# Performance work log

Hardware: AMD Instinct MI355X
Metric: run time of the kernel (lower is better)

The kernel has to match this reference:

```python
import jax, jax.numpy as jnp
import numpy as np

HEADS = 12
DIM_HEAD = 64
SCALE = DIM_HEAD ** -0.5


def setup_inputs() -> dict:
    key = jax.random.key(0)
    k1, k2, k3 = jax.random.split(key, 3)
    B, N, D = 4, 2048, 768
    inner = HEADS * DIM_HEAD  # 768
    x = jax.random.normal(k1, (B, N, D), dtype=jnp.float32)
    W_qkv = jax.random.normal(k2, (D, 3 * inner), dtype=jnp.float32) * (D ** -0.5)
    W_out = jax.random.normal(k3, (inner, D), dtype=jnp.float32) * (inner ** -0.5)
    b_out = jnp.zeros((D,), dtype=jnp.float32)
    return {"x": x, "W_qkv": W_qkv, "W_out": W_out, "b_out": b_out}


def reference(x, W_qkv, W_out, b_out):
    B, N, D = x.shape
    qkv = x @ W_qkv  # [B, N, 3*inner]
    q, k, v = jnp.split(qkv, 3, axis=-1)
    # 'b n (h d) -> b h n d'
    def split_heads(t):
        return t.reshape(B, N, HEADS, DIM_HEAD).transpose(0, 2, 1, 3)
    q, k, v = split_heads(q), split_heads(k), split_heads(v)
    dots = jnp.einsum('bhnd,bhmd->bhnm', q, k) * SCALE  # [B, H, N, N]
    attn = jax.nn.softmax(dots, axis=-1)
    out = jnp.einsum('bhnm,bhmd->bhnd', attn, v)
    out = out.transpose(0, 2, 1, 3).reshape(B, N, HEADS * DIM_HEAD)  # 'b h n d -> b n (h d)'
    return out @ W_out + b_out
```

## Files before the change

### kernel.cpp

```cpp
#include <hip/hip_runtime.h>
#include <hip/hip_bf16.h>

typedef __bf16 bf16_t;
typedef __bf16 bf16x4 __attribute__((ext_vector_type(4)));
typedef __bf16 bf16x8 __attribute__((ext_vector_type(8)));
typedef float f32x4 __attribute__((ext_vector_type(4)));
typedef float f32x16 __attribute__((ext_vector_type(16)));
typedef unsigned int u32x4 __attribute__((ext_vector_type(4)));

#define HEADS 12
#define DHEAD 64
#define NSEQ 2048
#define BATCH 4
#define DMODEL 768
#define NINNER 768

#define QSCALE 0.18033688011112042f

__device__ __forceinline__ void gl_lds16(const bf16_t* g, bf16_t* l) {
  __builtin_amdgcn_global_load_lds(
      (const __attribute__((address_space(1))) void*)g,
      (__attribute__((address_space(3))) void*)l, 16, 0, 0);
}

__device__ __forceinline__ unsigned pack_bf16_2(float a, float b) {
  unsigned lo = (unsigned)__builtin_bit_cast(unsigned short, (bf16_t)a);
  unsigned hi = (unsigned)__builtin_bit_cast(unsigned short, (bf16_t)b);
  return lo | (hi << 16);
}

__global__ void cast_bf16_kernel(const float* __restrict__ in, bf16_t* __restrict__ out, int n8) {
  int i = blockIdx.x * blockDim.x + threadIdx.x;
  const int stride = gridDim.x * blockDim.x;
  for (; i < n8; i += stride) {
    const f32x4* p = (const f32x4*)(in + (size_t)i * 8);
    f32x4 a = p[0], b = p[1];
    bf16x8 o;
#pragma unroll
    for (int j = 0; j < 4; ++j) { o[j] = (bf16_t)a[j]; o[j + 4] = (bf16_t)b[j]; }
    *(bf16x8*)(out + (size_t)i * 8) = o;
  }
}

__global__ void transpose_cast_kernel(const float* __restrict__ in, bf16_t* __restrict__ out,
                                      int K, int N) {
  __shared__ float tile[32][33];
  const int bx = blockIdx.x * 32;
  const int by = blockIdx.y * 32;
  const int tx = threadIdx.x, ty = threadIdx.y;
#pragma unroll
  for (int i = ty; i < 32; i += 8)
    tile[i][tx] = in[(size_t)(by + i) * N + bx + tx];
  __syncthreads();
#pragma unroll
  for (int i = ty; i < 32; i += 8)
    out[(size_t)(bx + i) * K + by + tx] = (bf16_t)tile[tx][i];
}

template <int MODE>
__global__ __launch_bounds__(256, 2)
void gemm_bt(const bf16_t* __restrict__ A, const bf16_t* __restrict__ Bt,
             bf16_t* __restrict__ qw, bf16_t* __restrict__ kw, bf16_t* __restrict__ vtw,
             const float* __restrict__ bias, float* __restrict__ outf,
             int M, int Nn, int K) {
  __shared__ bf16_t As[128 * 64];
  __shared__ bf16_t Bs[128 * 64];
  const int tid = threadIdx.x;
  const int wid = tid >> 6;
  const int lane = tid & 63;
  const int m0 = blockIdx.x * 128;
  const int n0 = blockIdx.y * 128;
  const int arow = lane >> 3;
  const int acol = (lane & 7) * 8;
  const int wm = (wid >> 1) * 64;
  const int wn = (wid & 1) * 64;
  const int fr = lane & 15;
  const int fg = lane >> 4;

  f32x4 acc[4][4] = {};

  for (int kt = 0; kt < K; kt += 64) {
    __syncthreads();
#pragma unroll
    for (int i = 0; i < 4; ++i) {
      const int c = i * 4 + wid;
      gl_lds16(A + (size_t)(m0 + c * 8 + arow) * K + kt + acol, As + c * 512);
      gl_lds16(Bt + (size_t)(n0 + c * 8 + arow) * K + kt + acol, Bs + c * 512);
    }
    __syncthreads();
#pragma unroll
    for (int kk = 0; kk < 2; ++kk) {
      bf16x8 af[4], bfr[4];
#pragma unroll
      for (int mi = 0; mi < 4; ++mi)
        af[mi] = *(const bf16x8*)(As + (wm + mi * 16 + fr) * 64 + kk * 32 + fg * 8);
#pragma unroll
      for (int ni = 0; ni < 4; ++ni)
        bfr[ni] = *(const bf16x8*)(Bs + (wn + ni * 16 + fr) * 64 + kk * 32 + fg * 8);
#pragma unroll
      for (int mi = 0; mi < 4; ++mi)
#pragma unroll
        for (int ni = 0; ni < 4; ++ni)
          acc[mi][ni] = __builtin_amdgcn_mfma_f32_16x16x32_bf16(af[mi], bfr[ni], acc[mi][ni], 0, 0, 0);
    }
  }

  if (MODE == 0 && n0 >= 2 * NINNER) {
#pragma unroll
    for (int mi = 0; mi < 4; ++mi) {
#pragma unroll
      for (int ni = 0; ni < 4; ++ni) {
        const int col = n0 + wn + ni * 16 + fr - 2 * NINNER;
        const int h = col >> 6, d = col & 63;
        const int row0 = m0 + wm + mi * 16 + fg * 4;
        const int b = row0 >> 11, n = row0 & 2047;
        bf16x4 pk;
#pragma unroll
        for (int r = 0; r < 4; ++r) pk[r] = (bf16_t)acc[mi][ni][r];
        *(bf16x4*)(vtw + ((size_t)((b * HEADS + h) * DHEAD + d)) * NSEQ + n) = pk;
      }
    }
  } else {
#pragma unroll
    for (int mi = 0; mi < 4; ++mi) {
#pragma unroll
      for (int ni = 0; ni < 4; ++ni) {
#pragma unroll
        for (int r = 0; r < 4; ++r) {
          const int row = m0 + wm + mi * 16 + fg * 4 + r;
          const int col = n0 + wn + ni * 16 + fr;
          float val = acc[mi][ni][r];
          if (MODE == 0) {
            const int which = col / NINNER;
            const int cin = col - which * NINNER;
            const int h = cin >> 6, d = cin & 63;
            const int b = row >> 11, n = row & 2047;
            bf16_t* dst = (which == 0) ? qw : kw;
            if (which == 0) val *= QSCALE;
            dst[(((size_t)(b * HEADS + h)) * NSEQ + n) * DHEAD + d] = (bf16_t)val;
          } else {
            outf[(size_t)row * Nn + col] = val + bias[col];
          }
        }
      }
    }
  }
}

__global__ __launch_bounds__(256, 3)
void attn_fwd(const bf16_t* __restrict__ qg, const bf16_t* __restrict__ kg,
              const bf16_t* __restrict__ vtg, bf16_t* __restrict__ og) {
  __shared__ bf16_t KV[2][16 * 512];
  const int tid = threadIdx.x, wid = tid >> 6, lane = tid & 63;
  const int logical = (blockIdx.x & 7) * 96 + (blockIdx.x >> 3);
  const int bh = logical >> 4;
  const int qbase = (logical & 15) * 128 + wid * 32;
  const bf16_t* Q = qg + (size_t)bh * NSEQ * DHEAD;
  const bf16_t* K = kg + (size_t)bh * NSEQ * DHEAD;
  const bf16_t* Vt = vtg + (size_t)bh * NSEQ * DHEAD;
  const int l31 = lane & 31, hi = lane >> 5;

  bf16x8 qf[4];
#pragma unroll
  for (int ks = 0; ks < 4; ++ks)
    qf[ks] = *(const bf16x8*)(Q + (size_t)(qbase + l31) * DHEAD + ks * 16 + hi * 8);

  f32x16 oacc[2] = {};
  float lsum = 0.f;

  auto stage = [&](int bsel, int t) {
    const int kv0 = t * 64;
#pragma unroll
    for (int i = 0; i < 4; ++i) {
      const int c = wid * 4 + i;
      bf16_t* dst = &KV[bsel][c * 512];
      if (c < 8) {
        gl_lds16(K + (size_t)(kv0 + (c >> 2) * 32 + l31) * DHEAD + (c & 3) * 16 + hi * 8, dst);
      } else {
        gl_lds16(Vt + (size_t)(((c >> 2) & 1) * 32 + l31) * NSEQ + kv0 + (c & 3) * 16 + hi * 8, dst);
      }
    }
  };

  stage(0, 0);

  for (int t = 0; t < NSEQ / 64; ++t) {
    const int buf = t & 1;
    asm volatile("s_waitcnt vmcnt(0) lgkmcnt(0)" ::: "memory");
    __builtin_amdgcn_sched_barrier(0);
    __syncthreads();
    if (t + 1 < NSEQ / 64) stage(buf ^ 1, t + 1);

    const bf16_t* base = &KV[buf][0];

    f32x16 sacc[2] = {};
    __builtin_amdgcn_s_setprio(1);
#pragma unroll
    for (int mi = 0; mi < 2; ++mi)
#pragma unroll
      for (int ks = 0; ks < 4; ++ks) {
        bf16x8 kf = *(const bf16x8*)(base + (mi * 4 + ks) * 512 + lane * 8);
        sacc[mi] = __builtin_amdgcn_mfma_f32_32x32x16_bf16(kf, qf[ks], sacc[mi], 0, 0, 0);
      }
    __builtin_amdgcn_s_setprio(0);

    bf16x8 pa[4];
#pragma unroll
    for (int mi = 0; mi < 2; ++mi) {
      float p[16];
#pragma unroll
      for (int r = 0; r < 16; ++r) p[r] = __builtin_amdgcn_exp2f(sacc[mi][r]);
      float rs = 0.f;
#pragma unroll
      for (int r = 0; r < 16; r += 4)
        rs += ((p[r] + p[r + 1]) + (p[r + 2] + p[r + 3]));
      lsum += rs;
      unsigned W[8];
#pragma unroll
      for (int j = 0; j < 8; ++j) W[j] = pack_bf16_2(p[2 * j], p[2 * j + 1]);
#pragma unroll
      for (int s = 0; s < 2; ++s) {
        const unsigned sendA = hi ? W[4 * s] : W[4 * s + 2];
        const unsigned sendB = hi ? W[4 * s + 1] : W[4 * s + 3];
        const unsigned recvA = __shfl_xor(sendA, 32, 64);
        const unsigned recvB = __shfl_xor(sendB, 32, 64);
        u32x4 pw;
        pw[0] = hi ? recvA : W[4 * s];
        pw[1] = hi ? recvB : W[4 * s + 1];
        pw[2] = hi ? W[4 * s + 2] : recvA;
        pw[3] = hi ? W[4 * s + 3] : recvB;
        pa[mi * 2 + s] = __builtin_bit_cast(bf16x8, pw);
      }
    }

    __builtin_amdgcn_s_setprio(1);
#pragma unroll
    for (int ni = 0; ni < 2; ++ni)
#pragma unroll
      for (int ks = 0; ks < 4; ++ks) {
        bf16x8 vf = *(const bf16x8*)(base + (8 + ni * 4 + ks) * 512 + lane * 8);
        oacc[ni] = __builtin_amdgcn_mfma_f32_32x32x16_bf16(pa[ks], vf, oacc[ni], 0, 0, 0);
      }
    __builtin_amdgcn_s_setprio(0);
  }

  lsum += __shfl_xor(lsum, 32, 64);
  const float inv0 = 1.0f / lsum;
  const int b = bh / HEADS, h = bh % HEADS;
#pragma unroll
  for (int r = 0; r < 16; ++r) {
    const int qq = (r & 3) + 8 * (r >> 2) + 4 * hi;
    const float invr = __shfl(inv0, qq, 64);
    const int n = qbase + qq;
#pragma unroll
    for (int ni = 0; ni < 2; ++ni)
      og[((size_t)b * NSEQ + n) * DMODEL + h * DHEAD + ni * 32 + l31] =
          (bf16_t)(oacc[ni][r] * invr);
  }
}

extern "C" void kernel_launch(void* const* d_in, const int* in_sizes, int n_in,
                              void* d_out, int out_size, void* d_ws, size_t ws_size,
                              hipStream_t stream) {
  const float* x    = (const float*)d_in[0];
  const float* Wqkv = (const float*)d_in[1];
  const float* Wout = (const float*)d_in[2];
  const float* bout = (const float*)d_in[3];
  float* out = (float*)d_out;

  char* ws = (char*)d_ws;
  bf16_t* xb    = (bf16_t*)(ws + 0);
  bf16_t* wqkvT = (bf16_t*)(ws + 12582912);
  bf16_t* woutT = (bf16_t*)(ws + 16121856);
  bf16_t* qw    = (bf16_t*)(ws + 17301504);
  bf16_t* kw    = (bf16_t*)(ws + 29884416);
  bf16_t* vtw   = (bf16_t*)(ws + 42467328);
  bf16_t* attno = (bf16_t*)(ws + 55050240);

  cast_bf16_kernel<<<1024, 256, 0, stream>>>(x, xb, (8192 * 768) / 8);
  transpose_cast_kernel<<<dim3(2304 / 32, 768 / 32), dim3(32, 8), 0, stream>>>(Wqkv, wqkvT, 768, 2304);
  transpose_cast_kernel<<<dim3(768 / 32, 768 / 32), dim3(32, 8), 0, stream>>>(Wout, woutT, 768, 768);

  gemm_bt<0><<<dim3(64, 18), 256, 0, stream>>>(xb, wqkvT, qw, kw, vtw, nullptr, nullptr,
                                               8192, 2304, 768);
  attn_fwd<<<768, 256, 0, stream>>>(qw, kw, vtw, attno);
  gemm_bt<1><<<dim3(64, 6), 256, 0, stream>>>(attno, woutT, nullptr, nullptr, nullptr, bout, out,
                                              8192, 768, 768);
}
```

Measured before the change: 157.4 us.

## Permute K rows to drop P shuffles and compute row sums via MFMA

K rows are loaded into LDS in a permuted (swizzled) order, so the S accumulator layout already matches the A-operand layout needed for the PV MFMA. This removes the cross-half lane shuffles that reorganized P. The per-lane row-sum adds and final shuffles are also replaced by an extra MFMA of P against a ones vector, which yields row sums in the output layout. The cost is four extra MFMAs per tile, and the row sums are now taken from bf16-rounded P instead of fp32 P.

```diff
diff --git a/kernel.cpp b/kernel.cpp
--- a/kernel.cpp
+++ b/kernel.cpp
@@ -159,14 +159,19 @@
   const bf16_t* K = kg + (size_t)bh * NSEQ * DHEAD;
   const bf16_t* Vt = vtg + (size_t)bh * NSEQ * DHEAD;
   const int l31 = lane & 31, hi = lane >> 5;
+  const int sw = (l31 & 19) | ((l31 & 4) << 1) | ((l31 & 8) >> 1);
 
   bf16x8 qf[4];
 #pragma unroll
   for (int ks = 0; ks < 4; ++ks)
     qf[ks] = *(const bf16x8*)(Q + (size_t)(qbase + l31) * DHEAD + ks * 16 + hi * 8);
 
+  bf16x8 onesf;
+#pragma unroll
+  for (int e = 0; e < 8; ++e) onesf[e] = (bf16_t)1.0f;
+
   f32x16 oacc[2] = {};
-  float lsum = 0.f;
+  f32x16 lacc = {};
 
   auto stage = [&](int bsel, int t) {
     const int kv0 = t * 64;
@@ -175,7 +180,7 @@
       const int c = wid * 4 + i;
       bf16_t* dst = &KV[bsel][c * 512];
       if (c < 8) {
-        gl_lds16(K + (size_t)(kv0 + (c >> 2) * 32 + l31) * DHEAD + (c & 3) * 16 + hi * 8, dst);
+        gl_lds16(K + (size_t)(kv0 + (c >> 2) * 32 + sw) * DHEAD + (c & 3) * 16 + hi * 8, dst);
       } else {
         gl_lds16(Vt + (size_t)(((c >> 2) & 1) * 32 + l31) * NSEQ + kv0 + (c & 3) * 16 + hi * 8, dst);
       }
@@ -210,25 +215,12 @@
       float p[16];
 #pragma unroll
       for (int r = 0; r < 16; ++r) p[r] = __builtin_amdgcn_exp2f(sacc[mi][r]);
-      float rs = 0.f;
-#pragma unroll
-      for (int r = 0; r < 16; r += 4)
-        rs += ((p[r] + p[r + 1]) + (p[r + 2] + p[r + 3]));
-      lsum += rs;
-      unsigned W[8];
-#pragma unroll
-      for (int j = 0; j < 8; ++j) W[j] = pack_bf16_2(p[2 * j], p[2 * j + 1]);
 #pragma unroll
       for (int s = 0; s < 2; ++s) {
-        const unsigned sendA = hi ? W[4 * s] : W[4 * s + 2];
-        const unsigned sendB = hi ? W[4 * s + 1] : W[4 * s + 3];
-        const unsigned recvA = __shfl_xor(sendA, 32, 64);
-        const unsigned recvB = __shfl_xor(sendB, 32, 64);
         u32x4 pw;
-        pw[0] = hi ? recvA : W[4 * s];
-        pw[1] = hi ? recvB : W[4 * s + 1];
-        pw[2] = hi ? W[4 * s + 2] : recvA;
-        pw[3] = hi ? W[4 * s + 3] : recvB;
+#pragma unroll
+        for (int w = 0; w < 4; ++w)
+          pw[w] = pack_bf16_2(p[8 * s + 2 * w], p[8 * s + 2 * w + 1]);
         pa[mi * 2 + s] = __builtin_bit_cast(bf16x8, pw);
       }
     }
@@ -241,16 +233,17 @@
         bf16x8 vf = *(const bf16x8*)(base + (8 + ni * 4 + ks) * 512 + lane * 8);
         oacc[ni] = __builtin_amdgcn_mfma_f32_32x32x16_bf16(pa[ks], vf, oacc[ni], 0, 0, 0);
       }
+#pragma unroll
+    for (int ks = 0; ks < 4; ++ks)
+      lacc = __builtin_amdgcn_mfma_f32_32x32x16_bf16(pa[ks], onesf, lacc, 0, 0, 0);
     __builtin_amdgcn_s_setprio(0);
   }
 
-  lsum += __shfl_xor(lsum, 32, 64);
-  const float inv0 = 1.0f / lsum;
   const int b = bh / HEADS, h = bh % HEADS;
 #pragma unroll
   for (int r = 0; r < 16; ++r) {
     const int qq = (r & 3) + 8 * (r >> 2) + 4 * hi;
-    const float invr = __shfl(inv0, qq, 64);
+    const float invr = 1.0f / lacc[r];
     const int n = qbase + qq;
 #pragma unroll
     for (int ni = 0; ni < 2; ++ni)
```

After: 151.6 us, median of 3. 3.7% less time.
